# Kernel optimization log

Measured on AMD Instinct MI355X. Metric: run time of the kernel, lower is better.

## Reference

```python
import jax, jax.numpy as jnp
import numpy as np

B, P, T, V, N, D = 16, 96, 128, 64, 16, 128


def setup_inputs() -> dict:
    key = jax.random.key(0)
    ks = jax.random.split(key, 9)
    s = 0.05  # weight scale for stability
    return {
        "queries": jax.random.normal(ks[0], (B, P, V, D), jnp.float32),
        "keys": jax.random.normal(ks[1], (B, T, V, D), jnp.float32),
        "var_ccc": jax.random.randint(ks[2], (B, V, N), 0, V),
        "Wq": jax.random.normal(ks[3], (D, D), jnp.float32) * s,
        "bq": jnp.zeros((D,), jnp.float32),
        "Wkv": jax.random.normal(ks[4], (D, D), jnp.float32) * s,
        "bkv": jnp.zeros((D,), jnp.float32),
        "Wout": jax.random.normal(ks[5], (D, D), jnp.float32) * s,
        "bout": jnp.zeros((D,), jnp.float32),
    }


def reference(queries, keys, var_ccc, Wq, bq, Wkv, bkv, Wout, bout):
    b, p, v, d = queries.shape
    scale = d ** -0.5
    # projections (nn.Linear: x @ W.T + b)
    q = queries @ Wq.T + bq                      # [B,P,V,D]
    k = keys @ Wkv.T + bkv                       # [B,T,V,D]
    k_last = k[:, -p:]                           # [B,P,V,D]
    # irregular gather of neighbor keys per (batch, variable)
    idx = var_ccc.reshape(b, -1)                 # [B, V*N]
    kc = jax.vmap(lambda kb, ib: kb[:, ib])(k_last, idx)  # [B,P,V*N,D]
    kc = kc.reshape(b, p, v, -1, d)              # [B,P,V,N,D] (keys == values)
    # tiny 1xN attention per (b,p,v)
    scores = jnp.einsum('bpvd,bpvnd->bpvn', q, kc) * scale
    attn = jax.nn.softmax(scores, axis=-1)       # dropout is identity in eval
    out = jnp.einsum('bpvn,bpvnd->bpvd', attn, kc)  # [B,P,V,D]
    res = jnp.concatenate([k[:, :-p], out], axis=1)  # [B,T,V,D]
    return res @ Wout.T + bout
```

## Files before the change

kernel.cpp:

```cpp
#include <hip/hip_runtime.h>

#define BB 16
#define PP 96
#define TT 128
#define VV 64
#define NN 16
#define DD 128
#define BPP (BB * PP)
#define NPASS (BB * 32)
#define SB 136
#define ST 72
#define SSF 68
#define SCALE 0.08838834764831845f
#define SLICE 4352

typedef __bf16 bf16x8 __attribute__((ext_vector_type(8)));
typedef __bf16 bf16x4 __attribute__((ext_vector_type(4)));
typedef float  floatx4 __attribute__((ext_vector_type(4)));
typedef unsigned int uint32x4 __attribute__((ext_vector_type(4)));

#define MFMA16(a, b, c) __builtin_amdgcn_mfma_f32_16x16x32_bf16(a, b, c, 0, 0, 0)

__device__ __forceinline__ bf16x8 cvt8(float4 a, float4 b) {
    return bf16x8{(__bf16)a.x, (__bf16)a.y, (__bf16)a.z, (__bf16)a.w,
                  (__bf16)b.x, (__bf16)b.y, (__bf16)b.z, (__bf16)b.w};
}

__device__ __forceinline__ void loadA_g(const float* Xs, int lm, int lq, bf16x8 af[4]) {
    const float4* p = (const float4*)(Xs + lm * DD + lq * 8);
#pragma unroll
    for (int ks = 0; ks < 4; ++ks) af[ks] = cvt8(p[8 * ks], p[8 * ks + 1]);
}

__device__ __forceinline__ void loadA_l(const __bf16* As, int sa, int lm, int lq,
                                        bf16x8* af, int kblocks) {
#pragma unroll
    for (int ks = 0; ks < 4; ++ks) {
        if (ks >= kblocks) break;
        af[ks] = *(const bf16x8*)(As + lm * sa + lq * 8 + 32 * ks);
    }
}

__device__ __forceinline__ void mmB(const bf16x8* af, const __bf16* B, int sb,
                                    int lm, int lq, floatx4* acc, int nblocks, int kblocks) {
#pragma unroll
    for (int nb = 0; nb < 8; ++nb) {
        if (nb >= nblocks) break;
        acc[nb] = floatx4{0.f, 0.f, 0.f, 0.f};
#pragma unroll
        for (int ks = 0; ks < 4; ++ks) {
            if (ks >= kblocks) break;
            bf16x8 bf = *(const bf16x8*)(B + (nb * 16 + lm) * sb + lq * 8 + 32 * ks);
            acc[nb] = MFMA16(af[ks], bf, acc[nb]);
        }
    }
}

__global__ void prep(const float* __restrict__ Wq, const float* __restrict__ Wkv,
                     const float* __restrict__ Wout, const float* __restrict__ bq,
                     const float* __restrict__ bkv, const float* __restrict__ bout,
                     __bf16* __restrict__ Wb, float* __restrict__ bcomb,
                     float* __restrict__ bqk) {
    int i = blockIdx.x, j = threadIdx.x;
    float m1 = 0.f, wc = 0.f;
    for (int k = 0; k < DD; ++k) {
        m1 += Wq[k * DD + j] * Wkv[k * DD + i];
        wc += Wout[i * DD + k] * Wkv[k * DD + j];
    }
    Wb[i * DD + j]         = (__bf16)m1;
    Wb[16384 + i * DD + j] = (__bf16)wc;
    if (i == 0) {
        float bs = bout[j], bk = 0.f;
        for (int k = 0; k < DD; ++k) {
            bs += Wout[j * DD + k] * bkv[k];
            bk += bq[k] * Wkv[k * DD + j];
        }
        bcomb[j] = bs;
        bqk[j] = bk;
    }
}

__global__ __launch_bounds__(256, 3) void fused(
    const float* __restrict__ queries, const float* __restrict__ keys,
    const int* __restrict__ ccc, const __bf16* __restrict__ Wb,
    const float* __restrict__ bqk, const float* __restrict__ bcomb,
    float* __restrict__ out) {
    __shared__ __align__(16) char lds[53248];
    __bf16* R1    = (__bf16*)lds;
    __bf16* smK   = (__bf16*)(lds + 17408);
    __bf16* smKCT = (__bf16*)(lds + 34816);
    float*  smS   = (float*)lds;

    int bl = blockIdx.x, t = threadIdx.x;
    int w = t >> 6, L = t & 63, lm = L & 15, lq = L >> 4;

    bf16x8 af[4];
    floatx4 acc[8];

    if (bl >= BPP) {
        int pb = bl - BPP;
        int b = pb >> 5, wi = pb & 31;
        const float* Xs = keys + ((long)b * TT * VV + wi * 64 + w * 16) * DD;
        float* Yg = out + ((long)b * TT * VV + wi * 64) * DD;
        loadA_g(Xs, lm, lq, af);
        mmB(af, Wb + 16384, DD, lm, lq, acc, 8, 4);
#pragma unroll
        for (int nb = 0; nb < 8; ++nb) {
            float bv = bcomb[nb * 16 + lm];
#pragma unroll
            for (int r = 0; r < 4; ++r)
                Yg[(long)(w * 16 + lq * 4 + r) * DD + nb * 16 + lm] = acc[nb][r] + bv;
        }
        return;
    }

    int b = bl / PP, p = bl % PP;
    const float* Qg = queries + ((long)(b * PP + p) * VV) * DD;
    const float* Kg = keys + ((long)(b * TT + 32 + p) * VV) * DD;
    float* Yg = out + ((long)(b * TT + 32 + p) * VV) * DD;

    float4 kr[8];
    {
        const float4* kp = (const float4*)(Kg + (w * 16 + lm) * DD + lq * 8);
#pragma unroll
        for (int ks = 0; ks < 4; ++ks) {
            kr[2 * ks] = kp[8 * ks]; kr[2 * ks + 1] = kp[8 * ks + 1];
        }
    }

#pragma unroll
    for (int ks = 0; ks < 4; ++ks) af[ks] = cvt8(kr[2 * ks], kr[2 * ks + 1]);
    mmB(af, Wb + 16384, DD, lm, lq, acc, 8, 4);

    float4 qr[8];
    {
        const float4* qp = (const float4*)(Qg + (w * 16 + lm) * DD + lq * 8);
#pragma unroll
        for (int ks = 0; ks < 4; ++ks) {
            qr[2 * ks] = qp[8 * ks]; qr[2 * ks + 1] = qp[8 * ks + 1];
        }
    }

#pragma unroll
    for (int ks = 0; ks < 4; ++ks)
        *(bf16x8*)(smK + (w * 16 + lm) * SB + lq * 8 + 32 * ks) = af[ks];

#pragma unroll
    for (int nb = 0; nb < 8; ++nb) {
        bf16x4 tp;
#pragma unroll
        for (int r = 0; r < 4; ++r) tp[r] = (__bf16)acc[nb][r];
        *(bf16x4*)(smKCT + (nb * 16 + lm) * ST + w * 16 + lq * 4) = tp;
    }

#pragma unroll
    for (int ks = 0; ks < 4; ++ks) af[ks] = cvt8(qr[2 * ks], qr[2 * ks + 1]);
    mmB(af, Wb, DD, lm, lq, acc, 8, 4);
#pragma unroll
    for (int nb = 0; nb < 8; ++nb) {
        float bv = bqk[nb * 16 + lm];
#pragma unroll
        for (int r = 0; r < 4; ++r)
            R1[(w * 16 + lq * 4 + r) * SB + nb * 16 + lm] = (__bf16)(acc[nb][r] + bv);
    }

    int se[NN];
    {
        const int4* cp = (const int4*)(ccc + ((long)b * VV + w * 16 + lm) * NN);
#pragma unroll
        for (int i = 0; i < 4; ++i) {
            int4 c4 = cp[i];
            se[4 * i] = c4.x; se[4 * i + 1] = c4.y;
            se[4 * i + 2] = c4.z; se[4 * i + 3] = c4.w;
        }
    }
    __syncthreads();

    loadA_l(R1 + w * 16 * SB, SB, lm, lq, af, 4);
    mmB(af, smK, SB, lm, lq, acc, 4, 4);
#pragma unroll
    for (int nb = 0; nb < 4; ++nb)
#pragma unroll
        for (int r = 0; r < 4; ++r)
            smS[(w * 16 + lq * 4 + r) * SSF + nb * 16 + lm] = acc[nb][r];

    __bf16* smAsl = (__bf16*)(lds + w * SLICE);
    {
        int g = lq;
        float sg[NN];
        const float* Srow = smS + (w * 16 + lm) * SSF;
#pragma unroll
        for (int n = 0; n < NN; ++n) sg[n] = Srow[se[n]];
        __builtin_amdgcn_sched_barrier(0);
        {
            uint32x4 z{0u, 0u, 0u, 0u};
            char* zb = (char*)smAsl + (L >> 2) * (ST * 2) + (L & 3) * 32;
            *(uint32x4*)zb = z;
            *(uint32x4*)(zb + 16) = z;
        }
        float mx = -1e30f;
#pragma unroll
        for (int n = 0; n < NN; ++n) { sg[n] *= SCALE; mx = fmaxf(mx, sg[n]); }
        float sum = 0.f;
#pragma unroll
        for (int n = 0; n < NN; ++n) { sg[n] = __expf(sg[n] - mx); sum += sg[n]; }
        float inv = 1.f / sum;
#pragma unroll
        for (int j = 0; j < 4; ++j) {
            int u = se[g * 4 + j];
            float tot = 0.f;
#pragma unroll
            for (int n = 0; n < NN; ++n) tot += (se[n] == u) ? sg[n] : 0.f;
            smAsl[lm * ST + u] = (__bf16)(tot * inv);
        }
    }

    loadA_l(smAsl, ST, lm, lq, af, 2);
    mmB(af, smKCT, ST, lm, lq, acc, 8, 2);
#pragma unroll
    for (int nb = 0; nb < 8; ++nb) {
        float bv = bcomb[nb * 16 + lm];
#pragma unroll
        for (int r = 0; r < 4; ++r)
            Yg[(long)(w * 16 + lq * 4 + r) * DD + nb * 16 + lm] = acc[nb][r] + bv;
    }
}

extern "C" void kernel_launch(void* const* d_in, const int* in_sizes, int n_in,
                              void* d_out, int out_size, void* d_ws, size_t ws_size,
                              hipStream_t stream) {
    const float* queries = (const float*)d_in[0];
    const float* keys    = (const float*)d_in[1];
    const int*   ccc     = (const int*)d_in[2];
    const float* Wq      = (const float*)d_in[3];
    const float* bq      = (const float*)d_in[4];
    const float* Wkv     = (const float*)d_in[5];
    const float* bkv     = (const float*)d_in[6];
    const float* Wout    = (const float*)d_in[7];
    const float* bout    = (const float*)d_in[8];
    float* out = (float*)d_out;

    __bf16* Wb    = (__bf16*)d_ws;
    float*  bcomb = (float*)((char*)d_ws + 65536);
    float*  bqk   = (float*)((char*)d_ws + 66048);

    prep<<<dim3(128), dim3(128), 0, stream>>>(Wq, Wkv, Wout, bq, bkv, bout, Wb, bcomb, bqk);

    fused<<<dim3(BPP + NPASS), dim3(256), 0, stream>>>(
        queries, keys, ccc, Wb, bqk, bcomb, out);
}
```

Baseline: 225.6 us.

## Alias smKCT onto smK to cut LDS and raise occupancy to four blocks

```diff
diff --git a/kernel.cpp b/kernel.cpp
--- a/kernel.cpp
+++ b/kernel.cpp
@@ -62,33 +62,39 @@
                      __bf16* __restrict__ Wb, float* __restrict__ bcomb,
                      float* __restrict__ bqk) {
     int i = blockIdx.x, j = threadIdx.x;
-    float m1 = 0.f, wc = 0.f;
-    for (int k = 0; k < DD; ++k) {
-        m1 += Wq[k * DD + j] * Wkv[k * DD + i];
-        wc += Wout[i * DD + k] * Wkv[k * DD + j];
-    }
-    Wb[i * DD + j]         = (__bf16)m1;
-    Wb[16384 + i * DD + j] = (__bf16)wc;
+    float m1[4] = {0.f, 0.f, 0.f, 0.f}, wc[4] = {0.f, 0.f, 0.f, 0.f};
+    for (int k = 0; k < DD; k += 4) {
+#pragma unroll
+        for (int u = 0; u < 4; ++u) {
+            m1[u] += Wq[(k + u) * DD + j] * Wkv[(k + u) * DD + i];
+            wc[u] += Wout[i * DD + k + u] * Wkv[(k + u) * DD + j];
+        }
+    }
+    Wb[i * DD + j]         = (__bf16)((m1[0] + m1[1]) + (m1[2] + m1[3]));
+    Wb[16384 + i * DD + j] = (__bf16)((wc[0] + wc[1]) + (wc[2] + wc[3]));
     if (i == 0) {
-        float bs = bout[j], bk = 0.f;
-        for (int k = 0; k < DD; ++k) {
-            bs += Wout[j * DD + k] * bkv[k];
-            bk += bq[k] * Wkv[k * DD + j];
-        }
-        bcomb[j] = bs;
-        bqk[j] = bk;
-    }
-}
-
-__global__ __launch_bounds__(256, 3) void fused(
+        float bs[4] = {bout[j], 0.f, 0.f, 0.f}, bk[4] = {0.f, 0.f, 0.f, 0.f};
+        for (int k = 0; k < DD; k += 4) {
+#pragma unroll
+            for (int u = 0; u < 4; ++u) {
+                bs[u] += Wout[j * DD + k + u] * bkv[k + u];
+                bk[u] += bq[k + u] * Wkv[(k + u) * DD + j];
+            }
+        }
+        bcomb[j] = (bs[0] + bs[1]) + (bs[2] + bs[3]);
+        bqk[j]   = (bk[0] + bk[1]) + (bk[2] + bk[3]);
+    }
+}
+
+__global__ __launch_bounds__(256, 4) void fused(
     const float* __restrict__ queries, const float* __restrict__ keys,
     const int* __restrict__ ccc, const __bf16* __restrict__ Wb,
     const float* __restrict__ bqk, const float* __restrict__ bcomb,
     float* __restrict__ out) {
-    __shared__ __align__(16) char lds[53248];
+    __shared__ __align__(16) char lds[35840];
     __bf16* R1    = (__bf16*)lds;
     __bf16* smK   = (__bf16*)(lds + 17408);
-    __bf16* smKCT = (__bf16*)(lds + 34816);
+    __bf16* smKCT = smK;
     float*  smS   = (float*)lds;
 
     int bl = blockIdx.x, t = threadIdx.x;
@@ -130,7 +136,11 @@
 
 #pragma unroll
     for (int ks = 0; ks < 4; ++ks) af[ks] = cvt8(kr[2 * ks], kr[2 * ks + 1]);
-    mmB(af, Wb + 16384, DD, lm, lq, acc, 8, 4);
+#pragma unroll
+    for (int ks = 0; ks < 4; ++ks)
+        *(bf16x8*)(smK + (w * 16 + lm) * SB + lq * 8 + 32 * ks) = af[ks];
+    floatx4 kc[8];
+    mmB(af, Wb + 16384, DD, lm, lq, kc, 8, 4);
 
     float4 qr[8];
     {
@@ -142,18 +152,6 @@
     }
 
 #pragma unroll
-    for (int ks = 0; ks < 4; ++ks)
-        *(bf16x8*)(smK + (w * 16 + lm) * SB + lq * 8 + 32 * ks) = af[ks];
-
-#pragma unroll
-    for (int nb = 0; nb < 8; ++nb) {
-        bf16x4 tp;
-#pragma unroll
-        for (int r = 0; r < 4; ++r) tp[r] = (__bf16)acc[nb][r];
-        *(bf16x4*)(smKCT + (nb * 16 + lm) * ST + w * 16 + lq * 4) = tp;
-    }
-
-#pragma unroll
     for (int ks = 0; ks < 4; ++ks) af[ks] = cvt8(qr[2 * ks], qr[2 * ks + 1]);
     mmB(af, Wb, DD, lm, lq, acc, 8, 4);
 #pragma unroll
@@ -163,6 +161,7 @@
         for (int r = 0; r < 4; ++r)
             R1[(w * 16 + lq * 4 + r) * SB + nb * 16 + lm] = (__bf16)(acc[nb][r] + bv);
     }
+    __syncthreads();
 
     int se[NN];
     {
@@ -174,7 +173,6 @@
             se[4 * i + 2] = c4.z; se[4 * i + 3] = c4.w;
         }
     }
-    __syncthreads();
 
     loadA_l(R1 + w * 16 * SB, SB, lm, lq, af, 4);
     mmB(af, smK, SB, lm, lq, acc, 4, 4);
@@ -183,6 +181,15 @@
 #pragma unroll
         for (int r = 0; r < 4; ++r)
             smS[(w * 16 + lq * 4 + r) * SSF + nb * 16 + lm] = acc[nb][r];
+    __syncthreads();
+
+#pragma unroll
+    for (int nb = 0; nb < 8; ++nb) {
+        bf16x4 tp;
+#pragma unroll
+        for (int r = 0; r < 4; ++r) tp[r] = (__bf16)kc[nb][r];
+        *(bf16x4*)(smKCT + (nb * 16 + lm) * ST + w * 16 + lq * 4) = tp;
+    }
 
     __bf16* smAsl = (__bf16*)(lds + w * SLICE);
     {
@@ -214,6 +221,7 @@
             smAsl[lm * ST + u] = (__bf16)(tot * inv);
         }
     }
+    __syncthreads();
 
     loadA_l(smAsl, ST, lm, lq, af, 2);
     mmB(af, smKCT, ST, lm, lq, acc, 8, 2);
```

Result: slower. 230.4 us (+2.1%).
